# Kernel optimization log

Measured on AMD Instinct MI355X. Metric: run time of the kernel, lower is better.

## Reference

```python
import jax, jax.numpy as jnp
from jax import lax
import numpy as np

HH = WW = 128          # backbone feature map (2048px image / stride 16)
C_IN = 512
FEAT_STRIDE = 16
N_ANCHOR = 9
NMS_THRESH = 0.7
N_PRE_NMS = 6000
N_POST_NMS = 300
MIN_SIZE = 16
NEG = jnp.float32(-1e30)


def _anchor_base(base_size=16, ratios=(0.5, 1.0, 2.0), scales=(8, 16, 32)):
    py = px = base_size / 2.0
    ab = np.zeros((len(ratios) * len(scales), 4), np.float32)
    for i, r in enumerate(ratios):
        for j, s in enumerate(scales):
            h = base_size * s * np.sqrt(r)
            w = base_size * s * np.sqrt(1.0 / r)
            ab[i * len(scales) + j] = [py - h / 2, px - w / 2, py + h / 2, px + w / 2]
    return ab


def _shifted_anchors(hh, ww):
    # (y1, x1, y2, x2) anchors enumerated row-major over (y, x), anchors innermost
    ab = _anchor_base()
    sy = np.arange(0, hh * FEAT_STRIDE, FEAT_STRIDE, dtype=np.float32)
    sx = np.arange(0, ww * FEAT_STRIDE, FEAT_STRIDE, dtype=np.float32)
    sx, sy = np.meshgrid(sx, sy)
    shift = np.stack((sy.ravel(), sx.ravel(), sy.ravel(), sx.ravel()), axis=1)
    anc = (ab[None, :, :] + shift[:, None, :]).reshape(-1, 4)
    return jnp.asarray(anc)


def _conv(x, w, b):
    y = lax.conv_general_dilated(x, w, (1, 1), 'SAME',
                                 dimension_numbers=('NHWC', 'HWIO', 'NHWC'))
    return y + b


def _loc2bbox(anchor, loc):
    sh = anchor[:, 2] - anchor[:, 0]
    sw = anchor[:, 3] - anchor[:, 1]
    scy = anchor[:, 0] + 0.5 * sh
    scx = anchor[:, 1] + 0.5 * sw
    cy = loc[:, 0] * sh + scy
    cx = loc[:, 1] * sw + scx
    h = jnp.exp(loc[:, 2]) * sh
    w = jnp.exp(loc[:, 3]) * sw
    return jnp.stack([cy - 0.5 * h, cx - 0.5 * w, cy + 0.5 * h, cx + 0.5 * w], axis=1)


def _nms(boxes, scores, thresh, n_out):
    # Greedy NMS with a fixed output size; invalid slots are zeroed.
    y1, x1, y2, x2 = boxes[:, 0], boxes[:, 1], boxes[:, 2], boxes[:, 3]
    areas = (y2 - y1) * (x2 - x1)

    def step(valid, _):
        s = jnp.where(valid, scores, NEG)
        i = jnp.argmax(s)
        ok = s[i] > NEG
        iy1 = jnp.maximum(y1, y1[i]); ix1 = jnp.maximum(x1, x1[i])
        iy2 = jnp.minimum(y2, y2[i]); ix2 = jnp.minimum(x2, x2[i])
        inter = jnp.maximum(iy2 - iy1, 0.0) * jnp.maximum(ix2 - ix1, 0.0)
        iou = inter / (areas + areas[i] - inter + 1e-9)
        valid = valid & (iou <= thresh)  # picked box suppresses itself (iou=1)
        return valid, (i, ok)

    _, (idx, oks) = lax.scan(step, jnp.ones(scores.shape, bool), None, length=n_out)
    return boxes[idx] * oks[:, None].astype(boxes.dtype)


def _proposals(loc, fg_score, anchor, img_h, img_w, scale):
    dst = _loc2bbox(anchor, loc)
    dst = jnp.stack([jnp.clip(dst[:, 0], 0.0, img_h),
                     jnp.clip(dst[:, 1], 0.0, img_w),
                     jnp.clip(dst[:, 2], 0.0, img_h),
                     jnp.clip(dst[:, 3], 0.0, img_w)], axis=1)
    min_size = MIN_SIZE * scale
    hs = dst[:, 2] - dst[:, 0]
    ws = dst[:, 3] - dst[:, 1]
    keep = (hs >= min_size) & (ws >= min_size)
    sc = jnp.where(keep, fg_score, -jnp.inf)
    top_s, top_i = lax.top_k(sc, N_PRE_NMS)
    return _nms(dst[top_i], top_s, NMS_THRESH, N_POST_NMS)


def _rpn_forward(x, conv_w, conv_b, loc_w, loc_b, score_w, score_b, img_h, img_w, scale):
    n, hh, ww, _ = x.shape
    anchor = _shifted_anchors(hh, ww)                    # [hh*ww*9, 4]
    h = jax.nn.relu(_conv(x, conv_w, conv_b))            # [n, hh, ww, 512]
    rpn_loc = _conv(h, loc_w, loc_b).reshape(n, -1, 4)   # [n, hh*ww*9, 4]
    rpn_score_map = _conv(h, score_w, score_b)           # [n, hh, ww, 18]
    soft = jax.nn.softmax(rpn_score_map.reshape(n, hh, ww, N_ANCHOR, 2), axis=-1)
    rpn_fg = soft[..., 1].reshape(n, -1)                 # [n, hh*ww*9]
    rpn_score = rpn_score_map.reshape(n, -1, 2)
    roi = _proposals(rpn_loc[0], rpn_fg[0], anchor, img_h, img_w, scale)  # [300, 4]
    return rpn_loc, rpn_score, roi, anchor


def setup_inputs() -> dict:
    key = jax.random.key(0)
    ks = jax.random.split(key, 4)
    return {
        "x": jax.random.normal(ks[0], (1, HH, WW, C_IN), jnp.float32),
        "conv_w": jax.random.normal(ks[1], (3, 3, C_IN, 512), jnp.float32) * 0.02,
        "conv_b": jnp.zeros((512,), jnp.float32),
        "loc_w": jax.random.normal(ks[2], (1, 1, 512, 36), jnp.float32) * 0.02,
        "loc_b": jnp.zeros((36,), jnp.float32),
        "score_w": jax.random.normal(ks[3], (1, 1, 512, 18), jnp.float32) * 0.02,
        "score_b": jnp.zeros((18,), jnp.float32),
        "img_h": HH * FEAT_STRIDE,
        "img_w": WW * FEAT_STRIDE,
        "scale": 1,
    }


def reference(x, conv_w, conv_b, loc_w, loc_b, score_w, score_b, img_h, img_w, scale):
    return _rpn_forward(x, conv_w, conv_b, loc_w, loc_b, score_w, score_b,
                        float(img_h), float(img_w), float(scale))
```

## Files before the change

kernel.cpp:

```cpp
#include <hip/hip_runtime.h>
#include <math.h>

typedef unsigned int u32;
typedef unsigned long long u64;
typedef _Float16 half8 __attribute__((ext_vector_type(8)));
typedef float f32x4 __attribute__((ext_vector_type(4)));
typedef float f32x16 __attribute__((ext_vector_type(16)));

#define N_PIX 16384
#define N_ANC 147456
#define N_PRE 6000
#define TIE_BASE 6144
#define TIE_CAP  16384

#define OFF_H      0ULL
#define OFF_BOXES  33554432ULL
#define OFF_KEYS   35913728ULL
#define OFF_W54    36503552ULL
#define OFF_B54    36634624ULL
#define OFF_HIST1  36634880ULL
#define OFF_HIST2  36897024ULL
#define OFF_CTRL   37159168ULL
#define OFF_CAND   37159424ULL
#define OFF_SBOX   37339648ULL
#define OFF_MASK   37437952ULL
#define BASE_NEEDED 41961984ULL
#define OFF_XH     41961984ULL
#define OFF_XL     58739200ULL
#define OFF_WHT    75516416ULL
#define OFF_WLT    80235008ULL
#define FULL_NEEDED 84953600ULL

#define KEY_NEGINF 0x007FFFFFu

#define MASK_BYTES 4524032ULL

struct AB { float v[36]; };


__device__ __forceinline__ void d_init_body(int i0, u32* hist1, u32* hist2, u32* ctrl, float* roi,
                       float* w54, float* b54,
                       const float* __restrict__ loc_w, const float* __restrict__ loc_b,
                       const float* __restrict__ score_w, const float* __restrict__ score_b) {
  const int stride = 256 * 256;
  const int TOT = 65536 * 2 + 64 + 1200 + 32768 + 64;
  for (int i = i0; i < TOT; i += stride) {
    if (i < 65536) hist1[i] = 0u;
    else if (i < 131072) hist2[i - 65536] = 0u;
    else if (i < 131136) ctrl[i - 131072] = 0u;
    else if (i < 132336) roi[i - 131136] = 0.f;
    else if (i < 165104) {
      int j = i - 132336;
      int k = j >> 6, oc = j & 63;
      float v = 0.f;
      if (oc < 36) v = loc_w[k * 36 + oc];
      else if (oc < 54) v = score_w[k * 18 + oc - 36];
      w54[(((k >> 2) << 6) + oc) * 4 + (k & 3)] = v;
    } else {
      int oc = i - 165104;
      float v = 0.f;
      if (oc < 36) v = loc_b[oc];
      else if (oc < 54) v = score_b[oc - 36];
      b54[oc] = v;
    }
  }
}

__device__ __forceinline__ void d_split_x_body(int b, int t, const float* __restrict__ x,
                                               _Float16* __restrict__ xh, _Float16* __restrict__ xl) {
  const int gid = b * 256 + t;
  const int base = gid << 3;
  float a[8];
  *(float4*)&a[0] = *(const float4*)(x + base);
  *(float4*)&a[4] = *(const float4*)(x + base + 4);
  half8 hh, ll;
#pragma unroll
  for (int j = 0; j < 8; ++j) {
    _Float16 hi = (_Float16)a[j];
    hh[j] = hi;
    ll[j] = (_Float16)((a[j] - (float)hi) * 2048.0f);
  }
  *(half8*)(xh + base) = hh;
  *(half8*)(xl + base) = ll;
}

__device__ __forceinline__ void d_split_w_body(int kb64, int ob, int t, const float* __restrict__ w,
                                               _Float16* __restrict__ whPK, _Float16* __restrict__ wlPK,
                                               _Float16 (*th)[72], _Float16 (*tl)[72]) {
  {
    const int r = t >> 2, cq = t & 3;
    float a[16];
    const float* wp = w + ((size_t)(kb64 * 64 + r) << 9) + ob * 64 + cq * 16;
#pragma unroll
    for (int j = 0; j < 4; ++j) *(float4*)&a[j << 2] = *(const float4*)(wp + (j << 2));
    half8 h0, h1, l0, l1;
#pragma unroll
    for (int j = 0; j < 8; ++j) {
      _Float16 hi = (_Float16)a[j];
      h0[j] = hi; l0[j] = (_Float16)((a[j] - (float)hi) * 2048.0f);
    }
#pragma unroll
    for (int j = 0; j < 8; ++j) {
      _Float16 hi = (_Float16)a[8 + j];
      h1[j] = hi; l1[j] = (_Float16)((a[8 + j] - (float)hi) * 2048.0f);
    }
    *(half8*)&th[r][cq * 16]     = h0;
    *(half8*)&th[r][cq * 16 + 8] = h1;
    *(half8*)&tl[r][cq * 16]     = l0;
    *(half8*)&tl[r][cq * 16 + 8] = l1;
  }
  __syncthreads();
  {
    const int o_local = t & 63;
    const int hl = (t >> 6) & 1;
    const int cs = t >> 7;
    const int tap = kb64 >> 3;
    const int ci  = ((kb64 & 7) << 1) + cs;
    const int kb  = ci * 9 + tap;
    const int o   = ob * 64 + o_local;
    const int nb  = o >> 7, n = o & 127;
    _Float16* dst = (hl ? wlPK : whPK) + (((size_t)(nb * 144 + kb)) << 12) + n * 8;
    _Float16 (*src)[72] = hl ? tl : th;
    const int r0 = cs << 5;
#pragma unroll
    for (int q = 0; q < 4; ++q) {
      half8 v;
#pragma unroll
      for (int j = 0; j < 8; ++j) v[j] = src[r0 + (q << 3) + j][o_local];
      *(half8*)(dst + (q << 10)) = v;
    }
  }
}

__global__ void k_init(u32* hist1, u32* hist2, u32* ctrl, float* roi,
                       float* w54, float* b54,
                       const float* __restrict__ loc_w, const float* __restrict__ loc_b,
                       const float* __restrict__ score_w, const float* __restrict__ score_b) {
  const int i0 = blockIdx.x * blockDim.x + threadIdx.x;
  d_init_body(i0, hist1, hist2, ctrl, roi, w54, b54, loc_w, loc_b, score_w, score_b);
}

__global__ __launch_bounds__(256) void k_prep(const float* __restrict__ x,
                                              _Float16* __restrict__ xh, _Float16* __restrict__ xl,
                                              const float* __restrict__ w,
                                              _Float16* __restrict__ whPK, _Float16* __restrict__ wlPK,
                                              u32* hist1, u32* hist2, u32* ctrl, float* roi,
                                              float* w54, float* b54,
                                              const float* __restrict__ loc_w, const float* __restrict__ loc_b,
                                              const float* __restrict__ score_w, const float* __restrict__ score_b) {
  __shared__ _Float16 th[64][72];
  __shared__ _Float16 tl[64][72];
  const int b = blockIdx.x;
  const int t = threadIdx.x;
  if (b < 4096) {
    d_split_x_body(b, t, x, xh, xl);
  } else if (b < 4672) {
    const int idx = b - 4096;
    d_split_w_body(idx % 72, idx / 72, t, w, whPK, wlPK, th, tl);
  } else {
    d_init_body((b - 4672) * 256 + t, hist1, hist2, ctrl, roi, w54, b54, loc_w, loc_b, score_w, score_b);
  }
}

__global__ __launch_bounds__(256, 2) void k_conv_pre(const _Float16* __restrict__ xh,
                                                     const _Float16* __restrict__ xl,
                                                     const _Float16* __restrict__ whPK,
                                                     const _Float16* __restrict__ wlPK,
                                                     const float* __restrict__ bias,
                                                     float* __restrict__ h) {
  __shared__ _Float16 As[2][3][4][130][8];

  const int bid = blockIdx.x;
  const int q   = bid >> 3;
  const int nb  = q >> 4;
  const int y   = ((bid & 7) << 4) + (q & 15);

  const int t  = threadIdx.x;
  const int wv = t >> 6, lane = t & 63;
  const int ln5 = lane & 31;
  const int kh  = lane >> 5;

  f32x16 acc_hh[4];
  f32x16 acc_x[4];
#pragma unroll
  for (int i = 0; i < 4; ++i) { acc_hh[i] = (f32x16)0.f; acc_x[i] = (f32x16)0.f; }

  const u32 wb = ((u32)kh << 10) + (((u32)((wv << 5) + ln5)) << 3);

  half8 bh0[2], bl0[2], bh1[2], bl1[2];

#define STAGE(CI)                                                                \
  {                                                                              \
    const int ch0_ = (CI) << 5;                                                  \
    _Pragma("unroll")                                                            \
    for (int j_ = 0; j_ < 13; ++j_) {                                            \
      const int c_ = t + (j_ << 8);                                              \
      if (c_ < 3120) {                                                           \
        const int p_ = c_ % 130;                                                 \
        int r_ = c_ / 130;                                                       \
        const int kq_ = r_ & 3; r_ >>= 2;                                        \
        const int ky_ = r_ % 3; const int hl_ = r_ / 3;                          \
        const int yy_ = y + ky_ - 1, xx_ = p_ - 1;                               \
        half8 v_ = (half8)(_Float16)0;                                           \
        if (yy_ >= 0 && yy_ < 128 && xx_ >= 0 && xx_ < 128) {                    \
          const _Float16* sp_ = (hl_ ? xl : xh) +                                \
              ((((size_t)((yy_ << 7) + xx_)) << 9) + ch0_ + (kq_ << 3));         \
          v_ = *(const half8*)sp_;                                               \
        }                                                                        \
        *(half8*)As[hl_][ky_][kq_][p_] = v_;                                     \
      }                                                                          \
    }                                                                            \
  }

#define BLOAD(KB, BH, BL)                                                        \
  {                                                                              \
    const u32 kbase_ = ((u32)(nb * 144 + (KB))) << 12;    \
    _Pragma("unroll")                                                            \
    for (int ks_ = 0; ks_ < 2; ++ks_) {                                          \
      const u32 o_ = kbase_ + ((u32)ks_ << 11) + wb;                             \
      BH[ks_] = *(const half8*)(whPK + o_);                                      \
      BL[ks_] = *(const half8*)(wlPK + o_);                                      \
    }                                                                            \
  }

#define FRAGS2(KYv, KXv, KS, AH, AL)                                             \
  {                                                                              \
    const int kq_ = ((KS) << 1) + kh;                                            \
    _Pragma("unroll")                                                            \
    for (int mi = 0; mi < 4; ++mi) {                                             \
      AH[mi] = *(const half8*)As[0][KYv][kq_][(mi << 5) + ln5 + (KXv)];          \
      AL[mi] = *(const half8*)As[1][KYv][kq_][(mi << 5) + ln5 + (KXv)];          \
    }                                                                            \
  }

#define MFMA12(AH, AL, BH, BL, KS)                                               \
  {                                                                              \
    _Pragma("unroll")                                                            \
    for (int mi = 0; mi < 4; ++mi) {                                             \
      acc_hh[mi] = __builtin_amdgcn_mfma_f32_32x32x16_f16(AH[mi], BH[KS], acc_hh[mi], 0, 0, 0); \
      acc_x[mi]  = __builtin_amdgcn_mfma_f32_32x32x16_f16(AH[mi], BL[KS], acc_x[mi], 0, 0, 0);  \
      acc_x[mi]  = __builtin_amdgcn_mfma_f32_32x32x16_f16(AL[mi], BH[KS], acc_x[mi], 0, 0, 0);  \
    }                                                                            \
  }

#define LBARRIER()                                                               \
  {                                                                              \
    asm volatile("s_waitcnt lgkmcnt(0)" ::: "memory");                           \
    __builtin_amdgcn_s_barrier();                                                \
  }

#define TAPSTEP(KYv, KXv, CUR, CURL, DO_PF, PFKB, NXT, NXTL)                     \
  {                                                                              \
    half8 a0h[4], a0l[4];                                                        \
    FRAGS2(KYv, KXv, 0, a0h, a0l);                                               \
    if (DO_PF) { BLOAD(PFKB, NXT, NXTL); }                                       \
    __builtin_amdgcn_sched_barrier(0);                                           \
    __builtin_amdgcn_s_setprio(1);                                               \
    MFMA12(a0h, a0l, CUR, CURL, 0);                                              \
    __builtin_amdgcn_s_setprio(0);                                               \
    half8 a1h[4], a1l[4];                                                        \
    FRAGS2(KYv, KXv, 1, a1h, a1l);                                               \
    __builtin_amdgcn_s_setprio(1);                                               \
    MFMA12(a1h, a1l, CUR, CURL, 1);                                              \
    __builtin_amdgcn_s_setprio(0);                                               \
  }

  BLOAD(0, bh0, bl0);
  STAGE(0);
  LBARRIER();

#pragma unroll 1
  for (int ci = 0; ci < 16; ++ci) {
    const int kb0 = ci * 9;
#pragma unroll 1
    for (int jp = 0; jp < 4; ++jp) {
      const int tp  = jp << 1;
      const int ky0 = tp / 3,       kx0 = tp - ky0 * 3;
      const int ky1 = (tp + 1) / 3, kx1 = (tp + 1) - ky1 * 3;
      TAPSTEP(ky0, kx0, bh0, bl0, true, kb0 + tp + 1, bh1, bl1)
      TAPSTEP(ky1, kx1, bh1, bl1, true, kb0 + tp + 2, bh0, bl0)
    }
    {
      const bool pf = (ci + 1 < 16);
      TAPSTEP(2, 2, bh0, bl0, pf, kb0 + 9, bh1, bl1)
    }
    if (ci + 1 < 16) {
#pragma unroll
      for (int k_ = 0; k_ < 2; ++k_) {
        bh0[k_] = bh1[k_];
        bl0[k_] = bl1[k_];
      }
      LBARRIER();
      STAGE(ci + 1);
      LBARRIER();
    }
  }
#undef STAGE
#undef BLOAD
#undef FRAGS2
#undef MFMA12
#undef LBARRIER
#undef TAPSTEP

  const float inv2048 = 1.0f / 2048.0f;
  const int colg = (nb << 7) + (wv << 5) + ln5;
  const float bbv = bias[colg];
#pragma unroll
  for (int mi = 0; mi < 4; ++mi) {
#pragma unroll
    for (int r = 0; r < 16; ++r) {
      const int row = (mi << 5) + (r & 3) + ((r >> 2) << 3) + (kh << 2);
      float v = acc_hh[mi][r] + acc_x[mi][r] * inv2048 + bbv;
      h[(((size_t)((y << 7) + row)) << 9) + colg] = fmaxf(v, 0.f);
    }
  }
}

#define APAD 40
__global__ __launch_bounds__(256, 2) void k_conv_fb(const float* __restrict__ x,
                                                    const float* __restrict__ w,
                                                    const float* __restrict__ bias,
                                                    float* __restrict__ h) {
  __shared__ _Float16 Ah[128][APAD];
  __shared__ _Float16 Al[128][APAD];
  __shared__ _Float16 Bh[128][APAD];
  __shared__ _Float16 Bl[128][APAD];

  const int y  = blockIdx.x;
  const int nb = blockIdx.y;
  const int t  = threadIdx.x;
  const int wv = t >> 6, lane = t & 63;
  const int m0 = (wv >> 1) << 6;
  const int n0 = (wv & 1) << 6;
  const int fm = lane & 15;
  const int fq = lane >> 4;
  const int sa_m = t >> 1;
  const int sa_h = (t & 1) << 4;
  const int sb_n = t & 127;
  const int sb_kg = (t >> 7) << 4;

  f32x4 acc_hh[4][4];
  f32x4 acc_x[4][4];
#pragma unroll
  for (int i = 0; i < 4; ++i)
#pragma unroll
    for (int j = 0; j < 4; ++j) { acc_hh[i][j] = (f32x4)0.f; acc_x[i][j] = (f32x4)0.f; }

#pragma unroll 1
  for (int kb = 0; kb < 144; ++kb) {
    const int tap  = kb >> 4;
    const int ky   = tap / 3, kx = tap - ky * 3;
    const int cin0 = (kb & 15) << 5;
    {
      const int yy = y + ky - 1;
      const int xx = sa_m + kx - 1;
      float av[16];
      if (yy >= 0 && yy < 128 && xx >= 0 && xx < 128) {
        const float* ap = x + (((size_t)((yy << 7) + xx)) << 9) + cin0 + sa_h;
#pragma unroll
        for (int j = 0; j < 4; ++j) *(float4*)&av[j << 2] = *(const float4*)(ap + (j << 2));
      } else {
#pragma unroll
        for (int j = 0; j < 16; ++j) av[j] = 0.f;
      }
      half8 h0, h1, l0, l1;
#pragma unroll
      for (int j = 0; j < 8; ++j) {
        _Float16 hi = (_Float16)av[j];
        h0[j] = hi; l0[j] = (_Float16)((av[j] - (float)hi) * 2048.0f);
      }
#pragma unroll
      for (int j = 0; j < 8; ++j) {
        _Float16 hi = (_Float16)av[8 + j];
        h1[j] = hi; l1[j] = (_Float16)((av[8 + j] - (float)hi) * 2048.0f);
      }
      *(half8*)&Ah[sa_m][sa_h]     = h0;
      *(half8*)&Ah[sa_m][sa_h + 8] = h1;
      *(half8*)&Al[sa_m][sa_h]     = l0;
      *(half8*)&Al[sa_m][sa_h + 8] = l1;
    }
    {
      const float* bp = w + ((size_t)(tap * 512 + cin0 + sb_kg) << 9) + (nb << 7) + sb_n;
      float bv[16];
#pragma unroll
      for (int j = 0; j < 16; ++j) bv[j] = bp[(size_t)j << 9];
      half8 h0, h1, l0, l1;
#pragma unroll
      for (int j = 0; j < 8; ++j) {
        _Float16 hi = (_Float16)bv[j];
        h0[j] = hi; l0[j] = (_Float16)((bv[j] - (float)hi) * 2048.0f);
      }
#pragma unroll
      for (int j = 0; j < 8; ++j) {
        _Float16 hi = (_Float16)bv[8 + j];
        h1[j] = hi; l1[j] = (_Float16)((bv[8 + j] - (float)hi) * 2048.0f);
      }
      *(half8*)&Bh[sb_n][sb_kg]     = h0;
      *(half8*)&Bh[sb_n][sb_kg + 8] = h1;
      *(half8*)&Bl[sb_n][sb_kg]     = l0;
      *(half8*)&Bl[sb_n][sb_kg + 8] = l1;
    }
    __syncthreads();
    half8 ah[4], al[4], bh[4], bl[4];
#pragma unroll
    for (int i = 0; i < 4; ++i) {
      ah[i] = *(const half8*)&Ah[m0 + (i << 4) + fm][fq << 3];
      al[i] = *(const half8*)&Al[m0 + (i << 4) + fm][fq << 3];
      bh[i] = *(const half8*)&Bh[n0 + (i << 4) + fm][fq << 3];
      bl[i] = *(const half8*)&Bl[n0 + (i << 4) + fm][fq << 3];
    }
#pragma unroll
    for (int mi = 0; mi < 4; ++mi)
#pragma unroll
      for (int ni = 0; ni < 4; ++ni) {
        acc_hh[mi][ni] = __builtin_amdgcn_mfma_f32_16x16x32_f16(ah[mi], bh[ni], acc_hh[mi][ni], 0, 0, 0);
        acc_x[mi][ni]  = __builtin_amdgcn_mfma_f32_16x16x32_f16(ah[mi], bl[ni], acc_x[mi][ni], 0, 0, 0);
        acc_x[mi][ni]  = __builtin_amdgcn_mfma_f32_16x16x32_f16(al[mi], bh[ni], acc_x[mi][ni], 0, 0, 0);
      }
    __syncthreads();
  }
  const float inv2048 = 1.0f / 2048.0f;
#pragma unroll
  for (int mi = 0; mi < 4; ++mi)
#pragma unroll
    for (int ni = 0; ni < 4; ++ni) {
      const int col = n0 + (ni << 4) + fm;
      const float bb = bias[(nb << 7) + col];
#pragma unroll
      for (int r = 0; r < 4; ++r) {
        const int row = m0 + (mi << 4) + (fq << 2) + r;
        float v = acc_hh[mi][ni][r] + acc_x[mi][ni][r] * inv2048 + bb;
        h[(((size_t)((y << 7) + row)) << 9) + (nb << 7) + col] = fmaxf(v, 0.f);
      }
    }
}

__global__ __launch_bounds__(256) void k_heads(const float* __restrict__ h,
        const float4* __restrict__ w54, const float* __restrict__ b54,
        float* __restrict__ out0, float* __restrict__ out1, float* __restrict__ out3,
        float4* __restrict__ boxes, u32* __restrict__ keys, u32* __restrict__ hist1,
        const int* __restrict__ p_ih, const int* __restrict__ p_iw,
        const int* __restrict__ p_sc, AB ab) {
  __shared__ float hl[16 * 512];
  __shared__ float vals[16][64];
  const int t = threadIdx.x;
  const int wv = t >> 6, lane = t & 63;
  const int pbase = blockIdx.x << 4;

#pragma unroll
  for (int j = 0; j < 8; ++j) {
    const int f = (j << 8) + t;
    ((float4*)hl)[f] = ((const float4*)(h + ((size_t)pbase << 9)))[f];
  }
  __syncthreads();

  const float* hp = hl + ((wv << 2) << 9);
  float a0 = 0.f, a1 = 0.f, a2 = 0.f, a3 = 0.f;
#pragma unroll 4
  for (int kq = 0; kq < 128; ++kq) {
    const float4 wvv = w54[(kq << 6) + lane];
    const float4 h0 = *(const float4*)(hp + (kq << 2));
    const float4 h1 = *(const float4*)(hp + 512 + (kq << 2));
    const float4 h2 = *(const float4*)(hp + 1024 + (kq << 2));
    const float4 h3 = *(const float4*)(hp + 1536 + (kq << 2));
    a0 += h0.x * wvv.x + h0.y * wvv.y + h0.z * wvv.z + h0.w * wvv.w;
    a1 += h1.x * wvv.x + h1.y * wvv.y + h1.z * wvv.z + h1.w * wvv.w;
    a2 += h2.x * wvv.x + h2.y * wvv.y + h2.z * wvv.z + h2.w * wvv.w;
    a3 += h3.x * wvv.x + h3.y * wvv.y + h3.z * wvv.z + h3.w * wvv.w;
  }
  const float bb = b54[lane];
  float av[4] = {a0 + bb, a1 + bb, a2 + bb, a3 + bb};
#pragma unroll
  for (int px = 0; px < 4; ++px) {
    const int p = pbase + (wv << 2) + px;
    vals[(wv << 2) + px][lane] = av[px];
    if (lane < 36) out0[p * 36 + lane] = av[px];
    else if (lane < 54) out1[p * 18 + lane - 36] = av[px];
  }
  __syncthreads();

  if (lane < 36) {
    const int px = lane / 9, a = lane - px * 9;
    const int p = pbase + (wv << 2) + px;
    const float* vv = vals[(wv << 2) + px];
    const float l0 = vv[(a << 2) + 0], l1 = vv[(a << 2) + 1];
    const float l2 = vv[(a << 2) + 2], l3 = vv[(a << 2) + 3];
    const float s0 = vv[36 + (a << 1)], s1 = vv[37 + (a << 1)];
    const int yq = p >> 7, xq = p & 127;
    const float fy = (float)(yq << 4), fx = (float)(xq << 4);
    const float ay1 = ab.v[(a << 2) + 0] + fy;
    const float ax1 = ab.v[(a << 2) + 1] + fx;
    const float ay2 = ab.v[(a << 2) + 2] + fy;
    const float ax2 = ab.v[(a << 2) + 3] + fx;
    const int idx = p * 9 + a;
    *(float4*)(out3 + ((size_t)idx << 2)) = make_float4(ay1, ax1, ay2, ax2);

    const float sh = ay2 - ay1, sw = ax2 - ax1;
    const float scy = ay1 + 0.5f * sh, scx = ax1 + 0.5f * sw;
    const float cy = l0 * sh + scy, cx = l1 * sw + scx;
    const float bh = expf(l2) * sh, bw = expf(l3) * sw;
    const float IH = (float)p_ih[0], IW = (float)p_iw[0];
    float d0 = fminf(fmaxf(cy - 0.5f * bh, 0.f), IH);
    float d1 = fminf(fmaxf(cx - 0.5f * bw, 0.f), IW);
    float d2 = fminf(fmaxf(cy + 0.5f * bh, 0.f), IH);
    float d3 = fminf(fmaxf(cx + 0.5f * bw, 0.f), IW);
    boxes[idx] = make_float4(d0, d1, d2, d3);

    const float minsz = 16.f * (float)p_sc[0];
    const bool keep = (d2 - d0 >= minsz) && (d3 - d1 >= minsz);
    const float mx = fmaxf(s0, s1);
    const float e0 = expf(s0 - mx), e1 = expf(s1 - mx);
    const float fg = e1 / (e0 + e1);
    const float sc = keep ? fg : -INFINITY;
    const u32 u = __float_as_uint(sc);
    const u32 key = (u & 0x80000000u) ? ~u : (u | 0x80000000u);
    keys[idx] = key;
    atomicAdd(&hist1[key >> 16], 1u);
  }
}

__global__ void k_hist2(const u32* __restrict__ keys, const u32* __restrict__ ctrl,
                        u32* __restrict__ hist2) {
  const u32 b1 = ctrl[0];
  int i = blockIdx.x * blockDim.x + threadIdx.x;
  if (i < N_ANC) {
    const u32 k = keys[i];
    if ((k >> 16) == b1) atomicAdd(&hist2[k & 0xFFFFu], 1u);
  }
}

__global__ __launch_bounds__(1024) void k_findcut(const u32* __restrict__ hist,
                                                  u32* __restrict__ ctrl, int mode) {
  __shared__ u32 csum[1024];
  __shared__ u32 suf[1024];
  const int t = threadIdx.x;
  const u32 target = (mode == 0) ? (u32)N_PRE : ((u32)N_PRE - ctrl[1]);
  const int base = t << 6;
  u32 s = 0;
  for (int i = 0; i < 64; ++i) s += hist[base + i];
  csum[t] = s;
  suf[t] = s;
  __syncthreads();
  for (int off = 1; off < 1024; off <<= 1) {
    u32 add = (t + off < 1024) ? suf[t + off] : 0u;
    __syncthreads();
    suf[t] += add;
    __syncthreads();
  }
  const u32 excl = suf[t] - csum[t];
  if (excl < target && target <= suf[t]) {
    u32 cum = excl;
    int bkt = base;
    for (int i = 63; i >= 0; --i) {
      const u32 hh = hist[base + i];
      if (cum < target && target <= cum + hh) { bkt = base + i; break; }
      cum += hh;
    }
    if (mode == 0) { ctrl[0] = (u32)bkt; ctrl[1] = cum; }
    else {
      const u32 Kstar = (ctrl[0] << 16) | (u32)bkt;
      const u32 A = ctrl[1] + cum;
      u32 need = (u32)N_PRE - A;
      if (Kstar == KEY_NEGINF) need = 0u;
      ctrl[2] = Kstar; ctrl[3] = A; ctrl[4] = need;
      ctrl[7] = A + need;
    }
  }
}

__global__ void k_compact(const u32* __restrict__ keys, u32* __restrict__ ctrl,
                          u64* __restrict__ cand) {
  const u32 Kstar = ctrl[2];
  const u32 need  = ctrl[4];
  int i = blockIdx.x * blockDim.x + threadIdx.x;
  if (i >= N_ANC) return;
  const u32 k = keys[i];
  if (k > Kstar) {
    const u32 pos = atomicAdd(&ctrl[5], 1u);
    cand[pos] = ((u64)k << 32) | (u64)(u32)(~(u32)i);
  } else if (k == Kstar && need != 0u) {
    const u32 pos = atomicAdd(&ctrl[6], 1u);
    if (pos < (u32)TIE_CAP) cand[TIE_BASE + pos] = ((u64)Kstar << 32) | (u64)(u32)(~(u32)i);
  }
}

__global__ __launch_bounds__(128) void k_rank(const u32* __restrict__ ctrl,
                                              const u64* __restrict__ cand,
                                              const float4* __restrict__ boxes,
                                              float4* __restrict__ sbox) {
  __shared__ u32 wred[2];
  const u32 A   = ctrl[3];
  const u32 tcc = min(ctrl[6], (u32)TIE_CAP);
  const u32 C   = A + tcc;
  const u32 L   = ctrl[7];
  const int t   = threadIdx.x;
  for (u32 i = blockIdx.x; i < C; i += gridDim.x) {
    const u64 v = (i < A) ? cand[i] : cand[TIE_BASE + (i - A)];
    u32 cnt = 0;
    for (u32 j = t; j < A; j += 128) cnt += (cand[j] > v);
    for (u32 j = t; j < tcc; j += 128) cnt += (cand[TIE_BASE + j] > v);
#pragma unroll
    for (int off = 32; off > 0; off >>= 1) cnt += __shfl_xor(cnt, off);
    if ((t & 63) == 0) wred[t >> 6] = cnt;
    __syncthreads();
    if (t == 0) {
      const u32 rank = wred[0] + wred[1];
      if (rank < L) {
        const u32 idx = ~((u32)(v & 0xFFFFFFFFULL));
        sbox[rank] = boxes[idx];
      }
    }
    __syncthreads();
  }
}

__global__ __launch_bounds__(256) void k_mask(const u32* __restrict__ ctrl,
                                              const float4* __restrict__ sbox,
                                              u64* __restrict__ mask) {
  const int L = (int)ctrl[7];
  const int rb = blockIdx.y;
  if (rb * 64 >= L) return;
  const int wv = threadIdx.x >> 6;
  const int lane = threadIdx.x & 63;
  const int cw = (blockIdx.x << 2) + wv;
  if (cw > 93 || cw < rb) return;
  const int j = cw * 64 + lane;
  const bool jok = (j < L);
  const float4 cb = jok ? sbox[j] : make_float4(0.f, 0.f, 0.f, 0.f);
  const float careaJ = (cb.z - cb.x) * (cb.w - cb.y);
  const int rbase = rb * 64;
  const float4 rbx = (rbase + lane < L) ? sbox[rbase + lane] : make_float4(0.f, 0.f, 0.f, 0.f);
  const int rmax = min(64, L - rbase);
  for (int r = 0; r < rmax; ++r) {
    const float ry1 = __shfl(rbx.x, r), rx1 = __shfl(rbx.y, r);
    const float ry2 = __shfl(rbx.z, r), rx2 = __shfl(rbx.w, r);
    const float ra = (ry2 - ry1) * (rx2 - rx1);
    const float iy1 = fmaxf(cb.x, ry1), ix1 = fmaxf(cb.y, rx1);
    const float iy2 = fminf(cb.z, ry2), ix2 = fminf(cb.w, rx2);
    const float inter = fmaxf(iy2 - iy1, 0.f) * fmaxf(ix2 - ix1, 0.f);
    const float iou = inter / (careaJ + ra - inter + 1e-9f);
    const bool bit = jok && (iou > 0.7f);
    const u64 bal = __ballot(bit);
    if (lane == 0) mask[(size_t)(rbase + r) * 94 + cw] = bal;
  }
}

__device__ inline u64 valid_mask_fn(int base, int L) {
  const int r = L - base;
  if (r <= 0) return 0ULL;
  if (r >= 64) return ~0ULL;
  return (1ULL << r) - 1ULL;
}
__device__ inline u64 above_mask_fn(int base, int i) {
  if (i < base) return ~0ULL;
  const int s = i - base + 1;
  if (s >= 64) return 0ULL;
  return (~0ULL) << s;
}

__device__ __forceinline__ void gload_lds16(const void* g, void* l) {
  __builtin_amdgcn_global_load_lds(
      (const __attribute__((address_space(1))) void*)g,
      (__attribute__((address_space(3))) void*)l, 16, 0, 0);
}

__global__ __launch_bounds__(64) void k_greedy(const u32* __restrict__ ctrl,
                                               const float* __restrict__ sboxf,
                                               const u64* __restrict__ mask,
                                               float* __restrict__ roi) {
  __shared__ char lds[4 * 12288];
  __shared__ float sbl[6144 * 4];
  const int lane = threadIdx.x;
  const int L = (int)ctrl[7];
  if (L <= 0) return;
  const char* gmask = (const char*)mask;
  const char* gend  = gmask + MASK_BYTES;
  const int nbatch = (L + 15) >> 4;

#pragma unroll 1
  for (int j = 0; j < 96; ++j)
    gload_lds16((const char*)sboxf + j * 1024 + lane * 16, (char*)sbl + j * 1024);

#define GISSUE(BB)                                                         \
  {                                                                        \
    const char* gb_ = gmask + (size_t)(BB) * 12032;                        \
    char* lb_ = lds + ((BB) & 3) * 12288;                                  \
    _Pragma("unroll")                                                      \
    for (int j_ = 0; j_ < 12; ++j_) {                                      \
      const char* ga_ = gb_ + j_ * 1024;                                   \
      if (ga_ + 1024 > gend) ga_ = gend - 1024;    \
      gload_lds16(ga_ + lane * 16, lb_ + j_ * 1024);                       \
    }                                                                      \
  }

  int next_issue = 0;
  int ready = -1;
  const int base0 = lane << 6;
  const int base1 = (64 + lane) << 6;
  const u64 v0 = valid_mask_fn(base0, L);
  const u64 v1 = (lane < 30) ? valid_mask_fn(base1, L) : 0ULL;
  u64 rem0 = 0ULL, rem1 = 0ULL;
  int i = 0, kept = 0;

  while (i >= 0 && kept < 300) {
    const int bi = i >> 4;
    if (bi > ready) {
      if (next_issue < bi) next_issue = bi;
      const int want = min(bi + 3, nbatch - 1);
      while (next_issue <= want) { GISSUE(next_issue); ++next_issue; }
      const int out = next_issue - 1 - bi;
      if (out >= 3)      asm volatile("s_waitcnt vmcnt(36)" ::: "memory");
      else if (out == 2) asm volatile("s_waitcnt vmcnt(24)" ::: "memory");
      else if (out == 1) asm volatile("s_waitcnt vmcnt(12)" ::: "memory");
      else               asm volatile("s_waitcnt vmcnt(0)"  ::: "memory");
      ready = bi;
    }
    if (lane < 4) roi[kept * 4 + lane] = sbl[(i << 2) + lane];
    ++kept;
    const u64* rowp = (const u64*)(lds + (bi & 3) * 12288 + (i & 15) * 752);
    rem0 |= rowp[lane];
    if (lane < 30) rem1 |= rowp[64 + lane];
    const u64 f0 = ~rem0 & v0 & above_mask_fn(base0, i);
    const u64 f1 = ~rem1 & v1 & above_mask_fn(base1, i);
    int ni = -1;
    const u64 b0 = __ballot(f0 != 0ULL);
    if (b0) {
      const int w = (int)__builtin_ctzll(b0);
      const u64 fw = (u64)__shfl((long long)f0, w);
      ni = (w << 6) + (int)__builtin_ctzll(fw);
    } else {
      const u64 b1m = __ballot(f1 != 0ULL);
      if (b1m) {
        const int w = (int)__builtin_ctzll(b1m);
        const u64 fw = (u64)__shfl((long long)f1, w);
        ni = ((64 + w) << 6) + (int)__builtin_ctzll(fw);
      }
    }
    i = ni;
  }
#undef GISSUE
}

extern "C" void kernel_launch(void* const* d_in, const int* in_sizes, int n_in,
                              void* d_out, int out_size, void* d_ws, size_t ws_size,
                              hipStream_t stream) {
  (void)in_sizes; (void)n_in; (void)out_size;
  if (ws_size < BASE_NEEDED) return;
  const bool fast = (ws_size >= FULL_NEEDED);

  const float* x       = (const float*)d_in[0];
  const float* conv_w  = (const float*)d_in[1];
  const float* conv_b  = (const float*)d_in[2];
  const float* loc_w   = (const float*)d_in[3];
  const float* loc_b   = (const float*)d_in[4];
  const float* score_w = (const float*)d_in[5];
  const float* score_b = (const float*)d_in[6];
  const int* p_ih = (const int*)d_in[7];
  const int* p_iw = (const int*)d_in[8];
  const int* p_sc = (const int*)d_in[9];

  float* out0 = (float*)d_out;
  float* out1 = out0 + 589824;
  float* roi  = out1 + 294912;
  float* out3 = roi + 1200;

  char* ws = (char*)d_ws;
  float*     h     = (float*)(ws + OFF_H);
  float4*    boxes = (float4*)(ws + OFF_BOXES);
  u32*       keys  = (u32*)(ws + OFF_KEYS);
  float*     w54   = (float*)(ws + OFF_W54);
  float*     b54   = (float*)(ws + OFF_B54);
  u32*       hist1 = (u32*)(ws + OFF_HIST1);
  u32*       hist2 = (u32*)(ws + OFF_HIST2);
  u32*       ctrl  = (u32*)(ws + OFF_CTRL);
  u64*       cand  = (u64*)(ws + OFF_CAND);
  float4*    sbox  = (float4*)(ws + OFF_SBOX);
  u64*       mask  = (u64*)(ws + OFF_MASK);
  _Float16*  xh    = (_Float16*)(ws + OFF_XH);
  _Float16*  xl    = (_Float16*)(ws + OFF_XL);
  _Float16*  whPK  = (_Float16*)(ws + OFF_WHT);
  _Float16*  wlPK  = (_Float16*)(ws + OFF_WLT);

  AB ab;
  {
    const double ratios[3] = {0.5, 1.0, 2.0};
    const double scales[3] = {8.0, 16.0, 32.0};
    for (int i = 0; i < 3; ++i)
      for (int j = 0; j < 3; ++j) {
        const double hh = 16.0 * scales[j] * sqrt(ratios[i]);
        const double wwv = 16.0 * scales[j] * sqrt(1.0 / ratios[i]);
        const int a = i * 3 + j;
        ab.v[a * 4 + 0] = (float)(8.0 - hh / 2.0);
        ab.v[a * 4 + 1] = (float)(8.0 - wwv / 2.0);
        ab.v[a * 4 + 2] = (float)(8.0 + hh / 2.0);
        ab.v[a * 4 + 3] = (float)(8.0 + wwv / 2.0);
      }
  }

  if (fast) {
    hipLaunchKernelGGL(k_prep, dim3(4928), dim3(256), 0, stream,
                       x, xh, xl, conv_w, whPK, wlPK,
                       hist1, hist2, ctrl, roi, w54, b54, loc_w, loc_b, score_w, score_b);
    hipLaunchKernelGGL(k_conv_pre, dim3(512), dim3(256), 0, stream, xh, xl, whPK, wlPK, conv_b, h);
  } else {
    hipLaunchKernelGGL(k_init, dim3(256), dim3(256), 0, stream,
                       hist1, hist2, ctrl, roi, w54, b54, loc_w, loc_b, score_w, score_b);
    hipLaunchKernelGGL(k_conv_fb, dim3(128, 4), dim3(256), 0, stream, x, conv_w, conv_b, h);
  }
  hipLaunchKernelGGL(k_heads, dim3(1024), dim3(256), 0, stream,
                     h, (const float4*)w54, b54, out0, out1, out3, boxes, keys, hist1,
                     p_ih, p_iw, p_sc, ab);
  hipLaunchKernelGGL(k_findcut, dim3(1), dim3(1024), 0, stream, hist1, ctrl, 0);
  hipLaunchKernelGGL(k_hist2, dim3(576), dim3(256), 0, stream, keys, ctrl, hist2);
  hipLaunchKernelGGL(k_findcut, dim3(1), dim3(1024), 0, stream, hist2, ctrl, 1);
  hipLaunchKernelGGL(k_compact, dim3(576), dim3(256), 0, stream, keys, ctrl, cand);
  hipLaunchKernelGGL(k_rank, dim3(8192), dim3(128), 0, stream, ctrl, cand, boxes, sbox);
  hipLaunchKernelGGL(k_mask, dim3(24, 94), dim3(256), 0, stream, ctrl, sbox, mask);
  hipLaunchKernelGGL(k_greedy, dim3(1), dim3(64), 0, stream, ctrl, (const float*)sbox, mask, roi);
}
```

Before: 628.0 us.

## Fuse post-heads selection, ranking, mask and greedy NMS into one cooperative kernel

Replaces the seven small kernels after the heads (two findcut passes, hist2, compact, rank, mask, greedy) with a single cooperative kernel of 256 blocks that uses grid.sync between phases. The goal is to remove per-launch overhead and idle gaps between tiny dependent kernels. In exchange, each phase now runs on only 256 blocks instead of the larger grids used before, with grid-wide barriers and atomic loads of ctrl. The findcut step is reworked for 256 threads with 256 buckets per thread.

```diff
diff --git a/kernel.cpp b/kernel.cpp
--- a/kernel.cpp
+++ b/kernel.cpp
@@ -1,5 +1,8 @@
 #include <hip/hip_runtime.h>
+#include <hip/hip_cooperative_groups.h>
 #include <math.h>
+
+namespace cg = cooperative_groups;
 
 typedef unsigned int u32;
 typedef unsigned long long u64;
@@ -37,6 +40,13 @@
 
 struct AB { float v[36]; };
 
+
+__device__ __forceinline__ u32 aload(const u32* p) {
+  return __hip_atomic_load(p, __ATOMIC_RELAXED, __HIP_MEMORY_SCOPE_AGENT);
+}
+__device__ __forceinline__ void astore(u32* p, u32 v) {
+  __hip_atomic_store(p, v, __ATOMIC_RELAXED, __HIP_MEMORY_SCOPE_AGENT);
+}
 
 __device__ __forceinline__ void d_init_body(int i0, u32* hist1, u32* hist2, u32* ctrl, float* roi,
                        float* w54, float* b54,
@@ -519,132 +529,6 @@
   }
 }
 
-__global__ void k_hist2(const u32* __restrict__ keys, const u32* __restrict__ ctrl,
-                        u32* __restrict__ hist2) {
-  const u32 b1 = ctrl[0];
-  int i = blockIdx.x * blockDim.x + threadIdx.x;
-  if (i < N_ANC) {
-    const u32 k = keys[i];
-    if ((k >> 16) == b1) atomicAdd(&hist2[k & 0xFFFFu], 1u);
-  }
-}
-
-__global__ __launch_bounds__(1024) void k_findcut(const u32* __restrict__ hist,
-                                                  u32* __restrict__ ctrl, int mode) {
-  __shared__ u32 csum[1024];
-  __shared__ u32 suf[1024];
-  const int t = threadIdx.x;
-  const u32 target = (mode == 0) ? (u32)N_PRE : ((u32)N_PRE - ctrl[1]);
-  const int base = t << 6;
-  u32 s = 0;
-  for (int i = 0; i < 64; ++i) s += hist[base + i];
-  csum[t] = s;
-  suf[t] = s;
-  __syncthreads();
-  for (int off = 1; off < 1024; off <<= 1) {
-    u32 add = (t + off < 1024) ? suf[t + off] : 0u;
-    __syncthreads();
-    suf[t] += add;
-    __syncthreads();
-  }
-  const u32 excl = suf[t] - csum[t];
-  if (excl < target && target <= suf[t]) {
-    u32 cum = excl;
-    int bkt = base;
-    for (int i = 63; i >= 0; --i) {
-      const u32 hh = hist[base + i];
-      if (cum < target && target <= cum + hh) { bkt = base + i; break; }
-      cum += hh;
-    }
-    if (mode == 0) { ctrl[0] = (u32)bkt; ctrl[1] = cum; }
-    else {
-      const u32 Kstar = (ctrl[0] << 16) | (u32)bkt;
-      const u32 A = ctrl[1] + cum;
-      u32 need = (u32)N_PRE - A;
-      if (Kstar == KEY_NEGINF) need = 0u;
-      ctrl[2] = Kstar; ctrl[3] = A; ctrl[4] = need;
-      ctrl[7] = A + need;
-    }
-  }
-}
-
-__global__ void k_compact(const u32* __restrict__ keys, u32* __restrict__ ctrl,
-                          u64* __restrict__ cand) {
-  const u32 Kstar = ctrl[2];
-  const u32 need  = ctrl[4];
-  int i = blockIdx.x * blockDim.x + threadIdx.x;
-  if (i >= N_ANC) return;
-  const u32 k = keys[i];
-  if (k > Kstar) {
-    const u32 pos = atomicAdd(&ctrl[5], 1u);
-    cand[pos] = ((u64)k << 32) | (u64)(u32)(~(u32)i);
-  } else if (k == Kstar && need != 0u) {
-    const u32 pos = atomicAdd(&ctrl[6], 1u);
-    if (pos < (u32)TIE_CAP) cand[TIE_BASE + pos] = ((u64)Kstar << 32) | (u64)(u32)(~(u32)i);
-  }
-}
-
-__global__ __launch_bounds__(128) void k_rank(const u32* __restrict__ ctrl,
-                                              const u64* __restrict__ cand,
-                                              const float4* __restrict__ boxes,
-                                              float4* __restrict__ sbox) {
-  __shared__ u32 wred[2];
-  const u32 A   = ctrl[3];
-  const u32 tcc = min(ctrl[6], (u32)TIE_CAP);
-  const u32 C   = A + tcc;
-  const u32 L   = ctrl[7];
-  const int t   = threadIdx.x;
-  for (u32 i = blockIdx.x; i < C; i += gridDim.x) {
-    const u64 v = (i < A) ? cand[i] : cand[TIE_BASE + (i - A)];
-    u32 cnt = 0;
-    for (u32 j = t; j < A; j += 128) cnt += (cand[j] > v);
-    for (u32 j = t; j < tcc; j += 128) cnt += (cand[TIE_BASE + j] > v);
-#pragma unroll
-    for (int off = 32; off > 0; off >>= 1) cnt += __shfl_xor(cnt, off);
-    if ((t & 63) == 0) wred[t >> 6] = cnt;
-    __syncthreads();
-    if (t == 0) {
-      const u32 rank = wred[0] + wred[1];
-      if (rank < L) {
-        const u32 idx = ~((u32)(v & 0xFFFFFFFFULL));
-        sbox[rank] = boxes[idx];
-      }
-    }
-    __syncthreads();
-  }
-}
-
-__global__ __launch_bounds__(256) void k_mask(const u32* __restrict__ ctrl,
-                                              const float4* __restrict__ sbox,
-                                              u64* __restrict__ mask) {
-  const int L = (int)ctrl[7];
-  const int rb = blockIdx.y;
-  if (rb * 64 >= L) return;
-  const int wv = threadIdx.x >> 6;
-  const int lane = threadIdx.x & 63;
-  const int cw = (blockIdx.x << 2) + wv;
-  if (cw > 93 || cw < rb) return;
-  const int j = cw * 64 + lane;
-  const bool jok = (j < L);
-  const float4 cb = jok ? sbox[j] : make_float4(0.f, 0.f, 0.f, 0.f);
-  const float careaJ = (cb.z - cb.x) * (cb.w - cb.y);
-  const int rbase = rb * 64;
-  const float4 rbx = (rbase + lane < L) ? sbox[rbase + lane] : make_float4(0.f, 0.f, 0.f, 0.f);
-  const int rmax = min(64, L - rbase);
-  for (int r = 0; r < rmax; ++r) {
-    const float ry1 = __shfl(rbx.x, r), rx1 = __shfl(rbx.y, r);
-    const float ry2 = __shfl(rbx.z, r), rx2 = __shfl(rbx.w, r);
-    const float ra = (ry2 - ry1) * (rx2 - rx1);
-    const float iy1 = fmaxf(cb.x, ry1), ix1 = fmaxf(cb.y, rx1);
-    const float iy2 = fminf(cb.z, ry2), ix2 = fminf(cb.w, rx2);
-    const float inter = fmaxf(iy2 - iy1, 0.f) * fmaxf(ix2 - ix1, 0.f);
-    const float iou = inter / (careaJ + ra - inter + 1e-9f);
-    const bool bit = jok && (iou > 0.7f);
-    const u64 bal = __ballot(bit);
-    if (lane == 0) mask[(size_t)(rbase + r) * 94 + cw] = bal;
-  }
-}
-
 __device__ inline u64 valid_mask_fn(int base, int L) {
   const int r = L - base;
   if (r <= 0) return 0ULL;
@@ -664,81 +548,221 @@
       (__attribute__((address_space(3))) void*)l, 16, 0, 0);
 }
 
-__global__ __launch_bounds__(64) void k_greedy(const u32* __restrict__ ctrl,
-                                               const float* __restrict__ sboxf,
-                                               const u64* __restrict__ mask,
-                                               float* __restrict__ roi) {
-  __shared__ char lds[4 * 12288];
-  __shared__ float sbl[6144 * 4];
-  const int lane = threadIdx.x;
-  const int L = (int)ctrl[7];
-  if (L <= 0) return;
-  const char* gmask = (const char*)mask;
-  const char* gend  = gmask + MASK_BYTES;
-  const int nbatch = (L + 15) >> 4;
+__device__ __forceinline__ void d_findcut256(const u32* hist, u32* ctrl, int mode,
+                                             u32* csum, u32* suf, int t) {
+  const u32 target = (mode == 0) ? (u32)N_PRE : ((u32)N_PRE - aload(&ctrl[1]));
+  const int base = t << 8;
+  u32 s = 0;
+  for (int i = 0; i < 256; ++i) s += aload(&hist[base + i]);
+  csum[t] = s;
+  suf[t] = s;
+  __syncthreads();
+  for (int off = 1; off < 256; off <<= 1) {
+    u32 add = (t + off < 256) ? suf[t + off] : 0u;
+    __syncthreads();
+    suf[t] += add;
+    __syncthreads();
+  }
+  const u32 excl = suf[t] - csum[t];
+  if (excl < target && target <= suf[t]) {
+    u32 cum = excl;
+    int bkt = base;
+    for (int i = 255; i >= 0; --i) {
+      const u32 hh = aload(&hist[base + i]);
+      if (cum < target && target <= cum + hh) { bkt = base + i; break; }
+      cum += hh;
+    }
+    if (mode == 0) { astore(&ctrl[0], (u32)bkt); astore(&ctrl[1], cum); }
+    else {
+      const u32 Kstar = (aload(&ctrl[0]) << 16) | (u32)bkt;
+      const u32 A = aload(&ctrl[1]) + cum;
+      u32 need = (u32)N_PRE - A;
+      if (Kstar == KEY_NEGINF) need = 0u;
+      astore(&ctrl[2], Kstar); astore(&ctrl[3], A); astore(&ctrl[4], need);
+      astore(&ctrl[7], A + need);
+    }
+  }
+}
+
+__global__ __launch_bounds__(256) void k_select(const u32* __restrict__ keys,
+                                                u32* hist1, u32* hist2, u32* ctrl,
+                                                u64* cand, const float4* __restrict__ boxes,
+                                                float4* sbox, u64* mask, float* roi) {
+  __shared__ char smem[147456];
+  cg::grid_group grid = cg::this_grid();
+  const int t = threadIdx.x;
+  const int b = blockIdx.x;
+
+  if (b == 0) d_findcut256(hist1, ctrl, 0, (u32*)smem, (u32*)(smem + 1024), t);
+  __threadfence();
+  grid.sync();
+
+  {
+    const u32 b1 = aload(&ctrl[0]);
+    for (int i = b * 256 + t; i < N_ANC; i += 65536) {
+      const u32 k = keys[i];
+      if ((k >> 16) == b1) atomicAdd(&hist2[k & 0xFFFFu], 1u);
+    }
+  }
+  __threadfence();
+  grid.sync();
+
+  if (b == 0) d_findcut256(hist2, ctrl, 1, (u32*)smem, (u32*)(smem + 1024), t);
+  __threadfence();
+  grid.sync();
+
+  {
+    const u32 Kstar = aload(&ctrl[2]);
+    const u32 need  = aload(&ctrl[4]);
+    for (int i = b * 256 + t; i < N_ANC; i += 65536) {
+      const u32 k = keys[i];
+      if (k > Kstar) {
+        const u32 pos = atomicAdd(&ctrl[5], 1u);
+        cand[pos] = ((u64)k << 32) | (u64)(u32)(~(u32)i);
+      } else if (k == Kstar && need != 0u) {
+        const u32 pos = atomicAdd(&ctrl[6], 1u);
+        if (pos < (u32)TIE_CAP) cand[TIE_BASE + pos] = ((u64)Kstar << 32) | (u64)(u32)(~(u32)i);
+      }
+    }
+  }
+  __threadfence();
+  grid.sync();
+
+  {
+    u32* wred = (u32*)smem;
+    const u32 A   = aload(&ctrl[3]);
+    const u32 tcc = min(aload(&ctrl[6]), (u32)TIE_CAP);
+    const u32 C   = A + tcc;
+    const u32 L   = aload(&ctrl[7]);
+    for (u32 i = (u32)b; i < C; i += 256) {
+      const u64 v = (i < A) ? cand[i] : cand[TIE_BASE + (i - A)];
+      u32 cnt = 0;
+      for (u32 j = t; j < A; j += 256) cnt += (cand[j] > v);
+      for (u32 j = t; j < tcc; j += 256) cnt += (cand[TIE_BASE + j] > v);
+#pragma unroll
+      for (int off = 32; off > 0; off >>= 1) cnt += __shfl_xor(cnt, off);
+      if ((t & 63) == 0) wred[t >> 6] = cnt;
+      __syncthreads();
+      if (t == 0) {
+        const u32 rank = wred[0] + wred[1] + wred[2] + wred[3];
+        if (rank < L) {
+          const u32 idx = ~((u32)(v & 0xFFFFFFFFULL));
+          sbox[rank] = boxes[idx];
+        }
+      }
+      __syncthreads();
+    }
+  }
+  __threadfence();
+  grid.sync();
+
+  {
+    const int L = (int)aload(&ctrl[7]);
+    const int wv = t >> 6;
+    const int lane = t & 63;
+    for (int pid = (b << 2) + wv; pid < 94 * 94; pid += 1024) {
+      const int rb = pid / 94;
+      const int cw = pid - rb * 94;
+      if (cw < rb || rb * 64 >= L) continue;
+      const int j = cw * 64 + lane;
+      const bool jok = (j < L);
+      const float4 cb = jok ? sbox[j] : make_float4(0.f, 0.f, 0.f, 0.f);
+      const float careaJ = (cb.z - cb.x) * (cb.w - cb.y);
+      const int rbase = rb * 64;
+      const float4 rbx = (rbase + lane < L) ? sbox[rbase + lane] : make_float4(0.f, 0.f, 0.f, 0.f);
+      const int rmax = min(64, L - rbase);
+      for (int r = 0; r < rmax; ++r) {
+        const float ry1 = __shfl(rbx.x, r), rx1 = __shfl(rbx.y, r);
+        const float ry2 = __shfl(rbx.z, r), rx2 = __shfl(rbx.w, r);
+        const float ra = (ry2 - ry1) * (rx2 - rx1);
+        const float iy1 = fmaxf(cb.x, ry1), ix1 = fmaxf(cb.y, rx1);
+        const float iy2 = fminf(cb.z, ry2), ix2 = fminf(cb.w, rx2);
+        const float inter = fmaxf(iy2 - iy1, 0.f) * fmaxf(ix2 - ix1, 0.f);
+        const float iou = inter / (careaJ + ra - inter + 1e-9f);
+        const bool bit = jok && (iou > 0.7f);
+        const u64 bal = __ballot(bit);
+        if (lane == 0) mask[(size_t)(rbase + r) * 94 + cw] = bal;
+      }
+    }
+  }
+  __threadfence();
+  grid.sync();
+
+  if (b != 0 || t >= 64) return;
+  {
+    char* lds = smem;
+    float* sbl = (float*)(smem + 49152);
+    const int lane = t;
+    const int L = (int)aload(&ctrl[7]);
+    if (L <= 0) return;
+    const char* gmask = (const char*)mask;
+    const char* gend  = gmask + MASK_BYTES;
+    const int nbatch = (L + 15) >> 4;
+    const float* sboxf = (const float*)sbox;
 
 #pragma unroll 1
-  for (int j = 0; j < 96; ++j)
-    gload_lds16((const char*)sboxf + j * 1024 + lane * 16, (char*)sbl + j * 1024);
+    for (int j = 0; j < 96; ++j)
+      gload_lds16((const char*)sboxf + j * 1024 + lane * 16, (char*)sbl + j * 1024);
 
 #define GISSUE(BB)                                                         \
-  {                                                                        \
-    const char* gb_ = gmask + (size_t)(BB) * 12032;                        \
-    char* lb_ = lds + ((BB) & 3) * 12288;                                  \
-    _Pragma("unroll")                                                      \
-    for (int j_ = 0; j_ < 12; ++j_) {                                      \
-      const char* ga_ = gb_ + j_ * 1024;                                   \
-      if (ga_ + 1024 > gend) ga_ = gend - 1024;    \
-      gload_lds16(ga_ + lane * 16, lb_ + j_ * 1024);                       \
-    }                                                                      \
-  }
-
-  int next_issue = 0;
-  int ready = -1;
-  const int base0 = lane << 6;
-  const int base1 = (64 + lane) << 6;
-  const u64 v0 = valid_mask_fn(base0, L);
-  const u64 v1 = (lane < 30) ? valid_mask_fn(base1, L) : 0ULL;
-  u64 rem0 = 0ULL, rem1 = 0ULL;
-  int i = 0, kept = 0;
-
-  while (i >= 0 && kept < 300) {
-    const int bi = i >> 4;
-    if (bi > ready) {
-      if (next_issue < bi) next_issue = bi;
-      const int want = min(bi + 3, nbatch - 1);
-      while (next_issue <= want) { GISSUE(next_issue); ++next_issue; }
-      const int out = next_issue - 1 - bi;
-      if (out >= 3)      asm volatile("s_waitcnt vmcnt(36)" ::: "memory");
-      else if (out == 2) asm volatile("s_waitcnt vmcnt(24)" ::: "memory");
-      else if (out == 1) asm volatile("s_waitcnt vmcnt(12)" ::: "memory");
-      else               asm volatile("s_waitcnt vmcnt(0)"  ::: "memory");
-      ready = bi;
-    }
-    if (lane < 4) roi[kept * 4 + lane] = sbl[(i << 2) + lane];
-    ++kept;
-    const u64* rowp = (const u64*)(lds + (bi & 3) * 12288 + (i & 15) * 752);
-    rem0 |= rowp[lane];
-    if (lane < 30) rem1 |= rowp[64 + lane];
-    const u64 f0 = ~rem0 & v0 & above_mask_fn(base0, i);
-    const u64 f1 = ~rem1 & v1 & above_mask_fn(base1, i);
-    int ni = -1;
-    const u64 b0 = __ballot(f0 != 0ULL);
-    if (b0) {
-      const int w = (int)__builtin_ctzll(b0);
-      const u64 fw = (u64)__shfl((long long)f0, w);
-      ni = (w << 6) + (int)__builtin_ctzll(fw);
-    } else {
-      const u64 b1m = __ballot(f1 != 0ULL);
-      if (b1m) {
-        const int w = (int)__builtin_ctzll(b1m);
-        const u64 fw = (u64)__shfl((long long)f1, w);
-        ni = ((64 + w) << 6) + (int)__builtin_ctzll(fw);
-      }
-    }
-    i = ni;
-  }
+    {                                                                      \
+      const char* gb_ = gmask + (size_t)(BB) * 12032;                      \
+      char* lb_ = lds + ((BB) & 3) * 12288;                                \
+      _Pragma("unroll")                                                    \
+      for (int j_ = 0; j_ < 12; ++j_) {                                    \
+        const char* ga_ = gb_ + j_ * 1024;                                 \
+        if (ga_ + 1024 > gend) ga_ = gend - 1024;                          \
+        gload_lds16(ga_ + lane * 16, lb_ + j_ * 1024);                     \
+      }                                                                    \
+    }
+
+    int next_issue = 0;
+    int ready = -1;
+    const int base0 = lane << 6;
+    const int base1 = (64 + lane) << 6;
+    const u64 v0 = valid_mask_fn(base0, L);
+    const u64 v1 = (lane < 30) ? valid_mask_fn(base1, L) : 0ULL;
+    u64 rem0 = 0ULL, rem1 = 0ULL;
+    int i = 0, kept = 0;
+
+    while (i >= 0 && kept < 300) {
+      const int bi = i >> 4;
+      if (bi > ready) {
+        if (next_issue < bi) next_issue = bi;
+        const int want = min(bi + 3, nbatch - 1);
+        while (next_issue <= want) { GISSUE(next_issue); ++next_issue; }
+        const int out = next_issue - 1 - bi;
+        if (out >= 3)      asm volatile("s_waitcnt vmcnt(36)" ::: "memory");
+        else if (out == 2) asm volatile("s_waitcnt vmcnt(24)" ::: "memory");
+        else if (out == 1) asm volatile("s_waitcnt vmcnt(12)" ::: "memory");
+        else               asm volatile("s_waitcnt vmcnt(0)"  ::: "memory");
+        ready = bi;
+      }
+      if (lane < 4) roi[kept * 4 + lane] = sbl[(i << 2) + lane];
+      ++kept;
+      const u64* rowp = (const u64*)(lds + (bi & 3) * 12288 + (i & 15) * 752);
+      rem0 |= rowp[lane];
+      if (lane < 30) rem1 |= rowp[64 + lane];
+      const u64 f0 = ~rem0 & v0 & above_mask_fn(base0, i);
+      const u64 f1 = ~rem1 & v1 & above_mask_fn(base1, i);
+      int ni = -1;
+      const u64 b0 = __ballot(f0 != 0ULL);
+      if (b0) {
+        const int w = (int)__builtin_ctzll(b0);
+        const u64 fw = (u64)__shfl((long long)f0, w);
+        ni = (w << 6) + (int)__builtin_ctzll(fw);
+      } else {
+        const u64 b1m = __ballot(f1 != 0ULL);
+        if (b1m) {
+          const int w = (int)__builtin_ctzll(b1m);
+          const u64 fw = (u64)__shfl((long long)f1, w);
+          ni = ((64 + w) << 6) + (int)__builtin_ctzll(fw);
+        }
+      }
+      i = ni;
+    }
 #undef GISSUE
+  }
 }
 
 extern "C" void kernel_launch(void* const* d_in, const int* in_sizes, int n_in,
@@ -810,11 +834,11 @@
   hipLaunchKernelGGL(k_heads, dim3(1024), dim3(256), 0, stream,
                      h, (const float4*)w54, b54, out0, out1, out3, boxes, keys, hist1,
                      p_ih, p_iw, p_sc, ab);
-  hipLaunchKernelGGL(k_findcut, dim3(1), dim3(1024), 0, stream, hist1, ctrl, 0);
-  hipLaunchKernelGGL(k_hist2, dim3(576), dim3(256), 0, stream, keys, ctrl, hist2);
-  hipLaunchKernelGGL(k_findcut, dim3(1), dim3(1024), 0, stream, hist2, ctrl, 1);
-  hipLaunchKernelGGL(k_compact, dim3(576), dim3(256), 0, stream, keys, ctrl, cand);
-  hipLaunchKernelGGL(k_rank, dim3(8192), dim3(128), 0, stream, ctrl, cand, boxes, sbox);
-  hipLaunchKernelGGL(k_mask, dim3(24, 94), dim3(256), 0, stream, ctrl, sbox, mask);
-  hipLaunchKernelGGL(k_greedy, dim3(1), dim3(64), 0, stream, ctrl, (const float*)sbox, mask, roi);
-}
+  {
+    const u32* keys_c = keys;
+    const float4* boxes_c = boxes;
+    void* args[] = {(void*)&keys_c, (void*)&hist1, (void*)&hist2, (void*)&ctrl,
+                    (void*)&cand, (void*)&boxes_c, (void*)&sbox, (void*)&mask, (void*)&roi};
+    hipLaunchCooperativeKernel((const void*)k_select, dim3(256), dim3(256), args, 0, stream);
+  }
+}
```

Measured after the change: 1.096 ms. 74.5% more time.
